# Optimization experiments

Measured on AMD Instinct MI355X. Metric: run time of the kernel, lower is better.

## Reference

```python
import jax, jax.numpy as jnp
import numpy as np

BATCH, N, DIM_IN, DIM_K, DIM_V, NH = 2, 4096, 256, 256, 256, 8

def setup_inputs() -> dict:
    key = jax.random.key(0)
    k1, k2, k3, k4 = jax.random.split(key, 4)
    s = 1.0 / np.sqrt(DIM_IN)
    return {
        "x": jax.random.normal(k1, (BATCH, N, DIM_IN), dtype=jnp.float32),
        "Wq": jax.random.normal(k2, (DIM_IN, DIM_K), dtype=jnp.float32) * s,
        "Wk": jax.random.normal(k3, (DIM_IN, DIM_K), dtype=jnp.float32) * s,
        "Wv": jax.random.normal(k4, (DIM_IN, DIM_V), dtype=jnp.float32) * s,
    }

def reference(x, Wq, Wk, Wv):
    b, n, _ = x.shape
    nh = NH
    dk = DIM_K // nh
    dv = DIM_V // nh
    # project and split heads: [b, nh, n, dk]
    q = jnp.einsum('bni,ik->bnk', x, Wq).reshape(b, n, nh, dk).transpose(0, 2, 1, 3)
    k = jnp.einsum('bni,ik->bnk', x, Wk).reshape(b, n, nh, dk).transpose(0, 2, 1, 3)
    v = jnp.einsum('bni,iv->bnv', x, Wv).reshape(b, n, nh, dv).transpose(0, 2, 1, 3)
    scale = 1.0 / np.sqrt(dk)
    dist = jnp.einsum('bhqd,bhkd->bhqk', q, k) * scale  # [b, nh, n, n]
    dist = jax.nn.softmax(dist, axis=-1)
    # dropout is identity in eval mode
    att = jnp.einsum('bhqk,bhkv->bhqv', dist, v)  # [b, nh, n, dv]
    return att.transpose(0, 2, 1, 3).reshape(b, n, DIM_V)
```

## Files before the change

kernel.cpp:

```cpp
#include <hip/hip_runtime.h>
#include <math.h>

#define BATCH 2
#define SEQ   4096
#define DIN   256
#define NH    8
#define DH    32
#define BH    (BATCH*NH)
#define QTILE 64
#define KPW   (SEQ/4)
#define ITERS (KPW/32)

typedef short bf16x8 __attribute__((ext_vector_type(8)));
typedef float f32x4  __attribute__((ext_vector_type(4)));

#if defined(__has_builtin)
#if __has_builtin(__builtin_amdgcn_exp2f)
#define EXP2(x) __builtin_amdgcn_exp2f(x)
#else
#define EXP2_ASM 1
#endif
#else
#define EXP2_ASM 1
#endif
#ifdef EXP2_ASM
__device__ __forceinline__ float exp2_raw(float x) {
    float r;
    asm("v_exp_f32 %0, %1\n\ts_nop 1" : "=v"(r) : "v"(x));
    return r;
}
#define EXP2(x) exp2_raw(x)
#endif

#define SC2 0.25508218f

__device__ __forceinline__ unsigned short f2bf(float f) {
    unsigned int u = __builtin_bit_cast(unsigned int, f);
    u += 0x7fffu + ((u >> 16) & 1u);
    return (unsigned short)(u >> 16);
}

__device__ __forceinline__ unsigned int pack_bf2(float f0, float f1) {
    unsigned int u0 = __builtin_bit_cast(unsigned int, f0) + 0x8000u;
    unsigned int u1 = __builtin_bit_cast(unsigned int, f1) + 0x8000u;
    return __builtin_amdgcn_perm(u1, u0, 0x07060302u);
}

__device__ __forceinline__ unsigned int pack_bf2_t(float f0, float f1) {
    return __builtin_amdgcn_perm(__builtin_bit_cast(unsigned int, f1),
                                 __builtin_bit_cast(unsigned int, f0),
                                 0x07060302u);
}

#if defined(__has_builtin)
#if __has_builtin(__builtin_amdgcn_global_load_lds)
#define HAS_ASYNC_LDS 1
#endif
#endif

__device__ __forceinline__ void stage16(const unsigned short* g,
                                        unsigned short* lds_base, int lane) {
#ifdef HAS_ASYNC_LDS
    __builtin_amdgcn_global_load_lds(
        (const __attribute__((address_space(1))) unsigned int*)g,
        (__attribute__((address_space(3))) unsigned int*)lds_base, 16, 0, 0);
#else
    *(bf16x8*)(lds_base + (size_t)lane * 8) = *(const bf16x8*)g;
#endif
}

__global__ __launch_bounds__(256) void prep_kernel(
    const float* __restrict__ Wq, const float* __restrict__ Wk, const float* __restrict__ Wv,
    unsigned short* __restrict__ Wt)
{
    __shared__ float ws[64][65];
    const int t = threadIdx.x;
    int wsel = blockIdx.x >> 4;
    int tile = blockIdx.x & 15;
    int tr = (tile >> 2) * 64;
    int tc = (tile & 3) * 64;
    const float* __restrict__ W = (wsel == 0) ? Wq : (wsel == 1) ? Wk : Wv;
    #pragma unroll
    for (int i = 0; i < 16; i++) {
        int row = i * 4 + (t >> 6), col = t & 63;
        ws[row][col] = W[(size_t)(tr + row) * DIN + tc + col];
    }
    __syncthreads();
    unsigned short* dst = Wt + (size_t)wsel * DIN * DIN;
    #pragma unroll
    for (int i = 0; i < 16; i++) {
        int orow = i * 4 + (t >> 6), ocol = t & 63;
        dst[(size_t)(tc + orow) * DIN + tr + ocol] = f2bf(ws[ocol][orow]);
    }
}

__global__ __launch_bounds__(256) void proj_kernel(
    const float* __restrict__ x, const unsigned short* __restrict__ Wt,
    unsigned short* __restrict__ qh, unsigned short* __restrict__ kh,
    unsigned short* __restrict__ vt)
{
    __shared__ __align__(16) unsigned short abuf[8][4][64][8];
    __shared__ __align__(16) unsigned short bbuf[8][4][64][8];

    const int wsel = blockIdx.y;
    const int w    = threadIdx.x >> 6;
    const int lane = threadIdx.x & 63;
    const int quad = lane >> 4;
    const int l16  = lane & 15;

    const int sl   = lane ^ (lane >> 3);
    const int sl16 = sl >> 2, squad = sl & 3;
    const int s_ = (l16 << 2) | quad;
    const int jj = (s_ & 56) | ((s_ ^ (s_ >> 3)) & 7);

    int arow0, brow0;
    const unsigned short* Wbase;
    const float* Xbase;
    unsigned short (*wdst)[4][64][8];
    unsigned short (*xdst)[4][64][8];
    if (wsel < 2) {
        int tt = blockIdx.x >> 7, nt = blockIdx.x & 127;
        arow0 = tt * 64; brow0 = nt * 64;
        Wbase = Wt + (size_t)wsel * DIN * DIN + (size_t)arow0 * DIN;
        Xbase = x + (size_t)brow0 * DIN;
        wdst = abuf; xdst = bbuf;
    } else {
        int nt = blockIdx.x >> 2, tt = blockIdx.x & 3;
        arow0 = nt * 64; brow0 = tt * 64;
        Xbase = x + (size_t)arow0 * DIN;
        Wbase = Wt + (size_t)2 * DIN * DIN + (size_t)brow0 * DIN;
        wdst = bbuf; xdst = abuf;
    }

    #pragma unroll
    for (int i = 0; i < 8; i++) {
        int id = w * 8 + i;
        int kb = id >> 2, rt = id & 3;
        stage16(Wbase + (size_t)(rt * 16 + sl16) * DIN + kb * 32 + squad * 8,
                &wdst[kb][rt][0][0], lane);
    }
    #pragma unroll
    for (int i = 0; i < 8; i++) {
        int id = w * 8 + i;
        int kb = id >> 2, rt = id & 3;
        const float4* src = (const float4*)(Xbase + (size_t)(rt * 16 + sl16) * DIN
                                            + kb * 32 + squad * 8);
        float4 a = src[0], b = src[1];
        uint4 p = { pack_bf2(a.x, a.y), pack_bf2(a.z, a.w),
                    pack_bf2(b.x, b.y), pack_bf2(b.z, b.w) };
        *(uint4*)(&xdst[kb][rt][0][0] + (size_t)lane * 8) = p;
    }
    __syncthreads();

    f32x4 acc[4];
    #pragma unroll
    for (int c = 0; c < 4; c++) acc[c] = (f32x4){0.f, 0.f, 0.f, 0.f};
    #pragma unroll
    for (int kb = 0; kb < 8; kb++) {
        bf16x8 af = *(const bf16x8*)&abuf[kb][w][jj][0];
        #pragma unroll
        for (int c = 0; c < 4; c++) {
            bf16x8 bfr = *(const bf16x8*)&bbuf[kb][c][jj][0];
            acc[c] = __builtin_amdgcn_mfma_f32_16x16x32_bf16(af, bfr, acc[c], 0, 0, 0);
        }
    }

    if (wsel < 2) {
        const float scl = (wsel == 0) ? SC2 : 1.0f;
        unsigned short* __restrict__ dst0 = (wsel == 0) ? qh : kh;
        const int t0 = arow0 + w * 16;
        const int h = t0 >> 5, d0 = (t0 & 31) + quad * 4;
        #pragma unroll
        for (int c = 0; c < 4; c++) {
            int n = brow0 + c * 16 + l16;
            int b = n >> 12, n12 = n & 4095;
            unsigned int u01 = pack_bf2(acc[c][0] * scl, acc[c][1] * scl);
            unsigned int u23 = pack_bf2(acc[c][2] * scl, acc[c][3] * scl);
            *(uint2*)&dst0[((size_t)(b * NH + h) * SEQ + n12) * DH + d0] = make_uint2(u01, u23);
        }
    } else {
        const int n0w = arow0 + w * 16;
        const int b = n0w >> 12, nbase = (n0w & 4095) + quad * 4;
        #pragma unroll
        for (int c = 0; c < 4; c++) {
            int t = brow0 + c * 16;
            int h = t >> 5, d = (t & 31) + l16;
            unsigned int u01 = pack_bf2(acc[c][0], acc[c][1]);
            unsigned int u23 = pack_bf2(acc[c][2], acc[c][3]);
            *(uint2*)&vt[((size_t)(b * NH + h) * DH + d) * SEQ + nbase] = make_uint2(u01, u23);
        }
    }
}

__global__ __launch_bounds__(256) void attn_kernel(
    const unsigned short* __restrict__ qh,
    const unsigned short* __restrict__ kh,
    const unsigned short* __restrict__ vt,
    float* __restrict__ out)
{
    __shared__ __align__(16) unsigned char smem[37888];
    unsigned short (*kbuf)[2][2][64][8] = (unsigned short (*)[2][2][64][8])smem;
    unsigned short (*vbuf)[2][2][64][8] = (unsigned short (*)[2][2][64][8])(smem + 16384);
    unsigned short (*pbuf)[16][40]      = (unsigned short (*)[16][40])(smem + 32768);

    const int tid  = threadIdx.x;
    const int wave = tid >> 6;
    const int lane = tid & 63;
    const int quad = lane >> 4;
    const int l16  = lane & 15;

    const int sl   = lane ^ (lane >> 3);
    const int sl16 = sl >> 2, squad = sl & 3;
    const int s_   = (l16 << 2) | quad;
    const int jj   = (s_ & 56) | ((s_ ^ (s_ >> 3)) & 7);

    const int bh = blockIdx.x & 15;
    const int qb = blockIdx.x >> 4;
    const int q0 = qb * QTILE;
    const int kstart = wave * KPW;

    const unsigned short* __restrict__ Qp = qh + (size_t)bh * SEQ * DH;
    const unsigned short* __restrict__ Kp = kh + (size_t)bh * SEQ * DH;
    const unsigned short* __restrict__ Vp = vt + (size_t)bh * DH * SEQ;

    bf16x8 qf[4];
    #pragma unroll
    for (int i = 0; i < 4; i++)
        qf[i] = *(const bf16x8*)(Qp + (size_t)(q0 + i * 16 + l16) * DH + quad * 8);

    const bf16x8 ones = {0x3F80, 0x3F80, 0x3F80, 0x3F80,
                         0x3F80, 0x3F80, 0x3F80, 0x3F80};

    f32x4 o[4][2];
    f32x4 lones[4];
    #pragma unroll
    for (int i = 0; i < 4; i++) {
        o[i][0] = (f32x4){0.f, 0.f, 0.f, 0.f};
        o[i][1] = (f32x4){0.f, 0.f, 0.f, 0.f};
        lones[i] = (f32x4){0.f, 0.f, 0.f, 0.f};
    }
    const f32x4 z = {0.f, 0.f, 0.f, 0.f};

    const unsigned short* ksrc0 = Kp + (size_t)(kstart +      sl16) * DH + squad * 8;
    const unsigned short* ksrc1 = Kp + (size_t)(kstart + 16 + sl16) * DH + squad * 8;
    const unsigned short* vsrc0 = Vp + (size_t)(     sl16) * SEQ + kstart + squad * 8;
    const unsigned short* vsrc1 = Vp + (size_t)(16 + sl16) * SEQ + kstart + squad * 8;

    stage16(ksrc0, &kbuf[wave][0][0][0][0], lane);
    stage16(ksrc1, &kbuf[wave][0][1][0][0], lane);
    stage16(vsrc0, &vbuf[wave][0][0][0][0], lane);
    stage16(vsrc1, &vbuf[wave][0][1][0][0], lane);
    ksrc0 += 32 * DH; ksrc1 += 32 * DH;
    vsrc0 += 32;      vsrc1 += 32;

    for (int t = 0; t < ITERS; t++) {
        const int buf = t & 1;

        __builtin_amdgcn_s_waitcnt(0x3F70);

        bf16x8 kf0 = *(const bf16x8*)&kbuf[wave][buf][0][jj][0];
        bf16x8 kf1 = *(const bf16x8*)&kbuf[wave][buf][1][jj][0];
        bf16x8 vf0 = *(const bf16x8*)&vbuf[wave][buf][0][jj][0];
        bf16x8 vf1 = *(const bf16x8*)&vbuf[wave][buf][1][jj][0];

        if (t + 1 < ITERS) {
            stage16(ksrc0, &kbuf[wave][buf ^ 1][0][0][0], lane);
            stage16(ksrc1, &kbuf[wave][buf ^ 1][1][0][0], lane);
            stage16(vsrc0, &vbuf[wave][buf ^ 1][0][0][0], lane);
            stage16(vsrc1, &vbuf[wave][buf ^ 1][1][0][0], lane);
            ksrc0 += 32 * DH; ksrc1 += 32 * DH;
            vsrc0 += 32;      vsrc1 += 32;
        }

        #pragma unroll
        for (int qt = 0; qt < 4; qt++) {
            f32x4 s0 = __builtin_amdgcn_mfma_f32_16x16x32_bf16(kf0, qf[qt], z, 0, 0, 0);
            f32x4 s1 = __builtin_amdgcn_mfma_f32_16x16x32_bf16(kf1, qf[qt], z, 0, 0, 0);
            #pragma unroll
            for (int c = 0; c < 2; c++) {
                const f32x4& s = c ? s1 : s0;
                float e0 = EXP2(s[0]);
                float e1 = EXP2(s[1]);
                float e2 = EXP2(s[2]);
                float e3 = EXP2(s[3]);
                *(uint2*)&pbuf[wave][l16][c * 16 + quad * 4] =
                    make_uint2(pack_bf2_t(e0, e1), pack_bf2_t(e2, e3));
            }
            bf16x8 pf = *(const bf16x8*)&pbuf[wave][l16][quad * 8];
            o[qt][0] = __builtin_amdgcn_mfma_f32_16x16x32_bf16(pf, vf0, o[qt][0], 0, 0, 0);
            o[qt][1] = __builtin_amdgcn_mfma_f32_16x16x32_bf16(pf, vf1, o[qt][1], 0, 0, 0);
            lones[qt] = __builtin_amdgcn_mfma_f32_16x16x32_bf16(pf, ones, lones[qt], 0, 0, 0);
        }
    }

    __syncthreads();
    unsigned short (*ored)[QTILE][40] = (unsigned short (*)[QTILE][40])smem;
    float (*lred)[QTILE] = (float (*)[QTILE])(smem + 32768);

    #pragma unroll
    for (int qt = 0; qt < 4; qt++) {
        #pragma unroll
        for (int r = 0; r < 4; r++) {
            int q = qt * 16 + quad * 4 + r;
            ored[wave][q][l16]      = f2bf(o[qt][0][r]);
            ored[wave][q][16 + l16] = f2bf(o[qt][1][r]);
            if (l16 == 0) lred[wave][q] = lones[qt][r];
        }
    }
    __syncthreads();

    const int b = bh >> 3, h = bh & 7;
    const int q  = tid >> 2;
    const int d0 = (tid & 3) * 8;
    float acc[8];
    #pragma unroll
    for (int j = 0; j < 8; j++) acc[j] = 0.f;
    #pragma unroll
    for (int w = 0; w < 4; w++) {
        uint4 v = *(const uint4*)&ored[w][q][d0];
        acc[0] += __builtin_bit_cast(float, v.x << 16);
        acc[1] += __builtin_bit_cast(float, v.x & 0xFFFF0000u);
        acc[2] += __builtin_bit_cast(float, v.y << 16);
        acc[3] += __builtin_bit_cast(float, v.y & 0xFFFF0000u);
        acc[4] += __builtin_bit_cast(float, v.z << 16);
        acc[5] += __builtin_bit_cast(float, v.z & 0xFFFF0000u);
        acc[6] += __builtin_bit_cast(float, v.w << 16);
        acc[7] += __builtin_bit_cast(float, v.w & 0xFFFF0000u);
    }
    float ls = (lred[0][q] + lred[1][q]) + (lred[2][q] + lred[3][q]);
    float inv = 1.f / ls;
    float* dst = out + ((size_t)b * SEQ + q0 + q) * (NH * DH) + h * DH + d0;
    float4 o0 = {acc[0] * inv, acc[1] * inv, acc[2] * inv, acc[3] * inv};
    float4 o1 = {acc[4] * inv, acc[5] * inv, acc[6] * inv, acc[7] * inv};
    ((float4*)dst)[0] = o0;
    ((float4*)dst)[1] = o1;
}

extern "C" void kernel_launch(void* const* d_in, const int* in_sizes, int n_in,
                              void* d_out, int out_size, void* d_ws, size_t ws_size,
                              hipStream_t stream)
{
    const float* x  = (const float*)d_in[0];
    const float* Wq = (const float*)d_in[1];
    const float* Wk = (const float*)d_in[2];
    const float* Wv = (const float*)d_in[3];
    float* out = (float*)d_out;

    unsigned short* qh = (unsigned short*)d_ws;
    unsigned short* kh = qh + (size_t)BH * SEQ * DH;
    unsigned short* vt = kh + (size_t)BH * SEQ * DH;
    unsigned short* Wt = vt + (size_t)BH * SEQ * DH;

    prep_kernel<<<dim3(48), 256, 0, stream>>>(Wq, Wk, Wv, Wt);
    proj_kernel<<<dim3(512, 3), 256, 0, stream>>>(x, Wt, qh, kh, vt);
    attn_kernel<<<dim3(BH * (SEQ / QTILE)), 256, 0, stream>>>(qh, kh, vt, out);
}
```

Before: 149.2 us.

## Deepen K/V prefetch to two tiles and double-buffer the P staging

Two K/V tiles are kept in flight by issuing the tile-after-next after each iteration's compute, with a relaxed vmcnt wait. The probability staging buffer is split into two alternating halves per wave, and the four exp2 calls per fragment are grouped under one asm block. The aim is to hide more global-load latency and cut wait stalls between the exp and MFMA phases. It costs more shared memory, and the unpadded P rows may cause LDS bank conflicts.

```diff
diff --git a/kernel.cpp b/kernel.cpp
--- a/kernel.cpp
+++ b/kernel.cpp
@@ -23,14 +23,22 @@
 #else
 #define EXP2_ASM 1
 #endif
+
+__device__ __forceinline__ void exp4(float& a, float& b, float& c, float& d) {
 #ifdef EXP2_ASM
-__device__ __forceinline__ float exp2_raw(float x) {
-    float r;
-    asm("v_exp_f32 %0, %1\n\ts_nop 1" : "=v"(r) : "v"(x));
-    return r;
-}
-#define EXP2(x) exp2_raw(x)
-#endif
+    float r0, r1, r2, r3;
+    asm("v_exp_f32 %0, %4\n\t"
+        "v_exp_f32 %1, %5\n\t"
+        "v_exp_f32 %2, %6\n\t"
+        "v_exp_f32 %3, %7\n\t"
+        "s_nop 1"
+        : "=&v"(r0), "=&v"(r1), "=&v"(r2), "=&v"(r3)
+        : "v"(a), "v"(b), "v"(c), "v"(d));
+    a = r0; b = r1; c = r2; d = r3;
+#else
+    a = EXP2(a); b = EXP2(b); c = EXP2(c); d = EXP2(d);
+#endif
+}
 
 #define SC2 0.25508218f
 
@@ -198,10 +206,10 @@
     const unsigned short* __restrict__ vt,
     float* __restrict__ out)
 {
-    __shared__ __align__(16) unsigned char smem[37888];
+    __shared__ __align__(16) unsigned char smem[40960];
     unsigned short (*kbuf)[2][2][64][8] = (unsigned short (*)[2][2][64][8])smem;
     unsigned short (*vbuf)[2][2][64][8] = (unsigned short (*)[2][2][64][8])(smem + 16384);
-    unsigned short (*pbuf)[16][40]      = (unsigned short (*)[16][40])(smem + 32768);
+    unsigned short (*pbuf)[2][16][32]   = (unsigned short (*)[2][16][32])(smem + 32768);
 
     const int tid  = threadIdx.x;
     const int wave = tid >> 6;
@@ -246,52 +254,55 @@
     const unsigned short* vsrc0 = Vp + (size_t)(     sl16) * SEQ + kstart + squad * 8;
     const unsigned short* vsrc1 = Vp + (size_t)(16 + sl16) * SEQ + kstart + squad * 8;
 
-    stage16(ksrc0, &kbuf[wave][0][0][0][0], lane);
-    stage16(ksrc1, &kbuf[wave][0][1][0][0], lane);
-    stage16(vsrc0, &vbuf[wave][0][0][0][0], lane);
-    stage16(vsrc1, &vbuf[wave][0][1][0][0], lane);
-    ksrc0 += 32 * DH; ksrc1 += 32 * DH;
-    vsrc0 += 32;      vsrc1 += 32;
+    #define ISSUE_TILE(B_)                                        \
+        do {                                                      \
+            stage16(ksrc0, &kbuf[wave][B_][0][0][0], lane);       \
+            stage16(ksrc1, &kbuf[wave][B_][1][0][0], lane);       \
+            stage16(vsrc0, &vbuf[wave][B_][0][0][0], lane);       \
+            stage16(vsrc1, &vbuf[wave][B_][1][0][0], lane);       \
+            ksrc0 += 32 * DH; ksrc1 += 32 * DH;                   \
+            vsrc0 += 32;      vsrc1 += 32;                        \
+        } while (0)
+
+    ISSUE_TILE(0);
+    ISSUE_TILE(1);
 
     for (int t = 0; t < ITERS; t++) {
         const int buf = t & 1;
 
-        __builtin_amdgcn_s_waitcnt(0x3F70);
+        if (t + 1 < ITERS)
+            __builtin_amdgcn_s_waitcnt(0x3F74);
+        else
+            __builtin_amdgcn_s_waitcnt(0x3F70);
 
         bf16x8 kf0 = *(const bf16x8*)&kbuf[wave][buf][0][jj][0];
         bf16x8 kf1 = *(const bf16x8*)&kbuf[wave][buf][1][jj][0];
         bf16x8 vf0 = *(const bf16x8*)&vbuf[wave][buf][0][jj][0];
         bf16x8 vf1 = *(const bf16x8*)&vbuf[wave][buf][1][jj][0];
 
-        if (t + 1 < ITERS) {
-            stage16(ksrc0, &kbuf[wave][buf ^ 1][0][0][0], lane);
-            stage16(ksrc1, &kbuf[wave][buf ^ 1][1][0][0], lane);
-            stage16(vsrc0, &vbuf[wave][buf ^ 1][0][0][0], lane);
-            stage16(vsrc1, &vbuf[wave][buf ^ 1][1][0][0], lane);
-            ksrc0 += 32 * DH; ksrc1 += 32 * DH;
-            vsrc0 += 32;      vsrc1 += 32;
-        }
-
         #pragma unroll
         for (int qt = 0; qt < 4; qt++) {
+            const int pr = qt & 1;
             f32x4 s0 = __builtin_amdgcn_mfma_f32_16x16x32_bf16(kf0, qf[qt], z, 0, 0, 0);
             f32x4 s1 = __builtin_amdgcn_mfma_f32_16x16x32_bf16(kf1, qf[qt], z, 0, 0, 0);
-            #pragma unroll
-            for (int c = 0; c < 2; c++) {
-                const f32x4& s = c ? s1 : s0;
-                float e0 = EXP2(s[0]);
-                float e1 = EXP2(s[1]);
-                float e2 = EXP2(s[2]);
-                float e3 = EXP2(s[3]);
-                *(uint2*)&pbuf[wave][l16][c * 16 + quad * 4] =
-                    make_uint2(pack_bf2_t(e0, e1), pack_bf2_t(e2, e3));
-            }
-            bf16x8 pf = *(const bf16x8*)&pbuf[wave][l16][quad * 8];
+            float e0 = s0[0], e1 = s0[1], e2 = s0[2], e3 = s0[3];
+            float e4 = s1[0], e5 = s1[1], e6 = s1[2], e7 = s1[3];
+            exp4(e0, e1, e2, e3);
+            exp4(e4, e5, e6, e7);
+            *(uint2*)&pbuf[wave][pr][l16][quad * 4] =
+                make_uint2(pack_bf2_t(e0, e1), pack_bf2_t(e2, e3));
+            *(uint2*)&pbuf[wave][pr][l16][16 + quad * 4] =
+                make_uint2(pack_bf2_t(e4, e5), pack_bf2_t(e6, e7));
+            bf16x8 pf = *(const bf16x8*)&pbuf[wave][pr][l16][quad * 8];
             o[qt][0] = __builtin_amdgcn_mfma_f32_16x16x32_bf16(pf, vf0, o[qt][0], 0, 0, 0);
             o[qt][1] = __builtin_amdgcn_mfma_f32_16x16x32_bf16(pf, vf1, o[qt][1], 0, 0, 0);
             lones[qt] = __builtin_amdgcn_mfma_f32_16x16x32_bf16(pf, ones, lones[qt], 0, 0, 0);
         }
-    }
+
+        if (t + 2 < ITERS)
+            ISSUE_TILE(buf);
+    }
+    #undef ISSUE_TILE
 
     __syncthreads();
     unsigned short (*ored)[QTILE][40] = (unsigned short (*)[QTILE][40])smem;
```

Result: slower. 170.9 us (+14.5%).
